# Kernel tuning notes

Hardware: AMD Instinct MI355X
Metric: run time of the kernel (lower is better)

The kernel has to match this reference:

```python
import jax, jax.numpy as jnp
import numpy as np

N_QUBITS = 13
DEPTH = 4
DIM = 2 ** N_QUBITS
PI = 3.141592653589793

# qubit 0 = most significant bit of the basis-state index
_idx = np.arange(DIM)
BITS = np.stack([(_idx >> (N_QUBITS - 1 - q)) & 1 for q in range(N_QUBITS)], axis=1)  # (DIM, n)
SIGNS = jnp.asarray(1.0 - 2.0 * BITS, dtype=jnp.float32)                               # Z eigenvalues, (DIM, n)
PARITY = jnp.asarray((-1.0) ** BITS.sum(axis=1), dtype=jnp.float32)                    # <Z^{(x)n}> diagonal, (DIM,)
# CZ entangling chain (q, q+1): diagonal (-1)^{sum_q b_q b_{q+1}}
ENT = jnp.asarray((-1.0) ** (BITS[:, :-1] * BITS[:, 1:]).sum(axis=1), dtype=jnp.float32)


def fwht(psi):
    """Normalized fast Walsh-Hadamard transform (H on every qubit), psi: (B, DIM) complex."""
    B = psi.shape[0]
    for q in range(N_QUBITS):
        psi = psi.reshape(B, 2 ** q, 2, -1)
        psi = jnp.stack([psi[:, :, 0] + psi[:, :, 1], psi[:, :, 0] - psi[:, :, 1]], axis=2)
    return psi.reshape(B, DIM) * (2.0 ** (-N_QUBITS / 2))


def feature_map_state(x):
    """Havlicek ZZ feature map: psi = D(x) H^n D(x) H^n |0...0>.
    Diagonal phase per basis state b: sum_j x_j s_j(b) + sum_{j<k} (pi-x_j)(pi-x_k) s_j(b) s_k(b)."""
    a = PI - x                                              # (B, n)
    u = x @ SIGNS.T                                         # (B, DIM)
    v = a @ SIGNS.T                                         # (B, DIM)
    phi = u + 0.5 * (v * v - jnp.sum(a * a, axis=1, keepdims=True))  # pair term via (sum)^2 trick
    d = jnp.exp(1j * phi)                                   # complex64 diagonal
    psi = jnp.full((x.shape[0], DIM), DIM ** -0.5, dtype=jnp.complex64)  # H^n |0>
    psi = fwht(d * psi)
    return d * psi


def _apply_1q(psi, U, q):
    """Apply 2x2 complex gate U to qubit q (bit-sliced)."""
    B = psi.shape[0]
    psi = psi.reshape(B, 2 ** q, 2, -1)
    a0, a1 = psi[:, :, 0], psi[:, :, 1]
    out = jnp.stack([U[0, 0] * a0 + U[0, 1] * a1, U[1, 0] * a0 + U[1, 1] * a1], axis=2)
    return out.reshape(B, DIM)


def variational_apply(psi, theta):
    """(DEPTH+1) layers of per-qubit Rz(b)Ry(a), CZ-chain entanglers between layers."""
    th = theta.reshape(DEPTH + 1, N_QUBITS, 2)
    for l in range(DEPTH + 1):
        if l > 0:
            psi = psi * ENT
        for q in range(N_QUBITS):
            ca = jnp.cos(0.5 * th[l, q, 0])
            sa = jnp.sin(0.5 * th[l, q, 0])
            em = jnp.exp(-0.5j * th[l, q, 1])
            ep = jnp.exp(0.5j * th[l, q, 1])
            U = jnp.stack([jnp.stack([em * ca, -em * sa]), jnp.stack([ep * sa, ep * ca])])
            psi = _apply_1q(psi, U, q)
    return psi


def setup_inputs() -> dict:
    key = jax.random.key(0)
    k1, k2 = jax.random.split(key)
    x = jax.random.normal(k1, (512, N_QUBITS), dtype=jnp.float32)
    theta = 0.1 * jax.random.normal(k2, ((DEPTH + 1) * N_QUBITS * 2,), dtype=jnp.float32)
    bias = jnp.zeros((1,), dtype=jnp.float32)
    return {"x": x, "theta": theta, "bias": bias}


def reference(x, theta, bias):
    psi = feature_map_state(x)
    psi = variational_apply(psi, theta)
    prob = psi.real ** 2 + psi.imag ** 2              # (B, DIM)
    logit = prob @ PARITY + bias[0]                   # (B,)
    return jnp.stack([-logit, logit], axis=1)         # two-class logits
```

## Files before the change

kernel.cpp:

```cpp
#include <hip/hip_runtime.h>
#include <hip/hip_fp16.h>

#define NQ   13
#define DIM  8192
#define PI_F 3.14159265358979323846f
#define NT   256
#define NAMP 32

#define NSLOT 9216

__device__ __forceinline__ int baseH(int t) { return 36 * t; }
__device__ __forceinline__ int baseL(int t) {
  int c = ((t & 1) << 7) | ((t & 2) << 5) | (t >> 2);
  return c + 4 * (c >> 5);
}

union F4H { float4 f; __half2 h[4]; };

__device__ __forceinline__ void rsincos(float x, float* s, float* c) {
  const float INV2PI = 0.15915494309189535f;
  const float TWOPI  = 6.283185307179586f;
  float r = x * INV2PI;
  r -= rintf(r);
  float ang = r * TWOPI;
  *s = __sinf(ang);
  *c = __cosf(ang);
}

__device__ __forceinline__ float2 f2fma(float s, float2 a, float2 b) {
  return make_float2(fmaf(s, a.x, b.x), fmaf(s, a.y, b.y));
}
__device__ __forceinline__ float2 f2add(float2 a, float2 b) {
  return make_float2(a.x + b.x, a.y + b.y);
}
__device__ __forceinline__ float2 f2sub(float2 a, float2 b) {
  return make_float2(a.x - b.x, a.y - b.y);
}
__device__ __forceinline__ float2 cphase(float2 v, float cs, float sn) {
  return make_float2(fmaf(cs, v.x, -sn * v.y), fmaf(cs, v.y, sn * v.x));
}
__device__ __forceinline__ float2 cmul(float2 a, float2 b) {
  return make_float2(fmaf(a.x, b.x, -a.y * b.y), fmaf(a.x, b.y, a.y * b.x));
}

template<int MASK>
__device__ __forceinline__ int xorLaneI(int x) {
  if constexpr (MASK == 1)
    return __builtin_amdgcn_update_dpp(x, x, 0xB1, 0xF, 0xF, false);
  else
    return __builtin_amdgcn_update_dpp(x, x, 0x4E, 0xF, 0xF, false);
}
template<int MASK>
__device__ __forceinline__ __half2 xorLaneH(__half2 v) {
  union { __half2 h; int i; } u; u.h = v;
  u.i = xorLaneI<MASK>(u.i);
  return u.h;
}

__device__ __forceinline__ void loadHh(const __half2* __restrict__ sAmp, int t, __half2* amp) {
  const __half2* p = sAmp + baseH(t);
  #pragma unroll
  for (int k = 0; k < 8; k++) {
    F4H u; u.f = *reinterpret_cast<const float4*>(p + 4 * k);
    #pragma unroll
    for (int c = 0; c < 4; c++) amp[4 * k + c] = u.h[c];
  }
}
__device__ __forceinline__ void storeHh(__half2* __restrict__ sAmp, int t, const __half2* amp) {
  __half2* p = sAmp + baseH(t);
  #pragma unroll
  for (int k = 0; k < 8; k++) {
    F4H u;
    #pragma unroll
    for (int c = 0; c < 4; c++) u.h[c] = amp[4 * k + c];
    *reinterpret_cast<float4*>(p + 4 * k) = u.f;
  }
}
__device__ __forceinline__ void loadLh(const __half2* __restrict__ sAmp, int t, __half2* amp) {
  const __half2* p = sAmp + baseL(t);
  #pragma unroll
  for (int j = 0; j < NAMP; j++) amp[j] = p[288 * j];
}
__device__ __forceinline__ void storeLh(__half2* __restrict__ sAmp, int t, const __half2* amp) {
  __half2* p = sAmp + baseL(t);
  #pragma unroll
  for (int j = 0; j < NAMP; j++) p[288 * j] = amp[j];
}

template<int KB>
__device__ __forceinline__ void fwht_bit(float2* amp) {
  #pragma unroll
  for (int j = 0; j < NAMP; j++) if (!(j & (1 << KB))) {
    int j1 = j | (1 << KB);
    float2 a0 = amp[j], a1 = amp[j1];
    amp[j]  = f2add(a0, a1);
    amp[j1] = f2sub(a0, a1);
  }
}
template<int KB>
__device__ __forceinline__ void applyRy(float2* amp, float ta, float sa) {
  #pragma unroll
  for (int j = 0; j < NAMP; j++) if (!(j & (1 << KB))) {
    int j1 = j | (1 << KB);
    amp[j]  = f2fma(-ta, amp[j1], amp[j]);
    amp[j1] = f2fma( sa, amp[j],  amp[j1]);
    amp[j]  = f2fma(-ta, amp[j1], amp[j]);
  }
}

template<int KB>
__device__ __forceinline__ void applyRyH(__half2* amp, __half2 nta, __half2 sa) {
  #pragma unroll
  for (int j = 0; j < NAMP; j++) if (!(j & (1 << KB))) {
    int j1 = j | (1 << KB);
    amp[j]  = __hfma2(nta, amp[j1], amp[j]);
    amp[j1] = __hfma2(sa,  amp[j],  amp[j1]);
    amp[j]  = __hfma2(nta, amp[j1], amp[j]);
  }
}

template<int MASK>
__device__ __forceinline__ void laneRyH(__half2* amp, __half2 c2, __half2 spm) {
  #pragma unroll
  for (int j = 0; j < NAMP; j++) {
    __half2 p = xorLaneH<MASK>(amp[j]);
    amp[j] = __hfma2(spm, p, __hmul2(c2, amp[j]));
  }
}
template<int MASK>
__device__ __forceinline__ void laneFwhtH(__half2* amp, __half2 sgn) {
  #pragma unroll
  for (int j = 0; j < NAMP; j++) {
    __half2 p = xorLaneH<MASK>(amp[j]);
    amp[j] = __hfma2(sgn, amp[j], p);
  }
}

template<int PAT>
__device__ __forceinline__ void buildTree(const float* __restrict__ w, float bias,
                                          int t, float* s) {
  float base = bias;
  if constexpr (PAT == 0) {
    #pragma unroll
    for (int k = 0; k < 8; k++) base += ((t >> k) & 1) ? w[5 + k] : 0.0f;
  } else {
    constexpr int BM[8] = {7, 6, 0, 1, 2, 3, 4, 5};
    #pragma unroll
    for (int k = 0; k < 8; k++) base += ((t >> k) & 1) ? w[BM[k]] : 0.0f;
  }
  constexpr int PH[5] = {0, 1, 2, 3, 4};
  constexpr int PL[5] = {8, 9, 10, 11, 12};
  s[0] = base;
  #pragma unroll
  for (int k = 0; k < 5; k++) {
    float wp = w[(PAT == 0) ? PH[k] : PL[k]];
    #pragma unroll
    for (int m = 0; m < (1 << k); m++) s[m | (1 << k)] = s[m] + wp;
  }
}

template<int PAT, bool INIT>
__device__ __forceinline__ void featureDiag(float2* amp,
                                            const float* __restrict__ wXp,
                                            const float* __restrict__ wAp,
                                            const float* __restrict__ consp, int t) {
  float u[NAMP], v[NAMP];
  buildTree<PAT>(wXp, consp[0], t, u);
  buildTree<PAT>(wAp, consp[1], t, v);
  float A2 = consp[2];
  #pragma unroll
  for (int j = 0; j < NAMP; j++) {
    float phi = u[j] + 0.5f * (v[j] * v[j] - A2);
    float sn, cs; rsincos(phi, &sn, &cs);
    if constexpr (INIT) amp[j] = make_float2(cs, sn);
    else                amp[j] = cphase(amp[j], cs, sn);
  }
}

template<int PAT>
__device__ __forceinline__ void applyDiag(float2* amp,
                                          const float* __restrict__ wb,
                                          const float* __restrict__ eR,
                                          const float* __restrict__ eI,
                                          float bias, int t) {
  float base = bias;
  if constexpr (PAT == 0) {
    #pragma unroll
    for (int k = 0; k < 8; k++) base += ((t >> k) & 1) ? wb[5 + k] : 0.0f;
  } else {
    constexpr int BM[8] = {7, 6, 0, 1, 2, 3, 4, 5};
    #pragma unroll
    for (int k = 0; k < 8; k++) base += ((t >> k) & 1) ? wb[BM[k]] : 0.0f;
  }
  constexpr int E0 = (PAT == 0) ? 0 : 8;
  const int ct = (PAT == 0) ? 0 : (((t & 1) << 7) | ((t & 2) << 5) | (t >> 2));
  float2 c[16];
  { float sn, cs; rsincos(base, &sn, &cs); c[0] = make_float2(cs, sn); }
  #pragma unroll
  for (int k = 0; k < 4; k++) {
    float2 e = make_float2(eR[E0 + k], eI[E0 + k]);
    #pragma unroll
    for (int m = 0; m < (1 << k); m++) c[m | (1 << k)] = cmul(c[m], e);
  }
  #pragma unroll
  for (int j = 0; j < 16; j++) {
    int i = (PAT == 0) ? ((t << 5) | j) : ((j << 8) | ct);
    float sgn = (__popc(i & (i >> 1)) & 1) ? -1.0f : 1.0f;
    amp[j] = cphase(amp[j], c[j].x * sgn, c[j].y * sgn);
  }
  float2 e4 = make_float2(eR[E0 + 4], eI[E0 + 4]);
  #pragma unroll
  for (int j = 16; j < 32; j++) {
    int i = (PAT == 0) ? ((t << 5) | j) : ((j << 8) | ct);
    float sgn = (__popc(i & (i >> 1)) & 1) ? -1.0f : 1.0f;
    float2 cc = cmul(c[j - 16], e4);
    amp[j] = cphase(amp[j], cc.x * sgn, cc.y * sgn);
  }
}

__global__ __launch_bounds__(NT, 1) void qc_kernel(
    const float* __restrict__ xin,
    const float* __restrict__ thin,
    const float* __restrict__ bin,
    float* __restrict__ out) {
  __shared__ alignas(16) __half2 sAmp[NSLOT];
  __shared__ float gTA[65], gSA[65];
  __shared__ __half2 hNTA[65], hSA[65];
  __shared__ __half2 hC2[65], hS2[65];
  __shared__ float gBbit[65];
  __shared__ float eBr[65], eBi[65];
  __shared__ float wX[13], wA[13];
  __shared__ float cons[8];
  __shared__ float red[NT / 64];

  const int t = threadIdx.x;
  const int lane = t & 63;
  const int b = blockIdx.x;

  if (t < NQ) {
    float xq = xin[b * NQ + t];
    float aq = PI_F - xq;
    wX[12 - t] = -2.0f * xq;
    wA[12 - t] = -2.0f * aq;
  }
  if (t < 65) {
    float av = thin[2 * t];
    float bv = thin[2 * t + 1];
    float ca = cosf(0.5f * av);
    float sa = sinf(0.5f * av);
    float ta = sa / (1.0f + ca);
    gTA[t] = ta;
    gSA[t] = sa;
    hNTA[t] = __float2half2_rn(-ta);
    hSA[t]  = __float2half2_rn(sa);
    hC2[t]  = __float2half2_rn(ca);
    hS2[t]  = __float2half2_rn(sa);
    int l = t / NQ, q = t % NQ;
    int s = l * NQ + (12 - q);
    gBbit[s] = bv;
    eBr[s] = cosf(bv);
    eBi[s] = sinf(bv);
  }
  __syncthreads();
  if (t == 0) {
    float X = 0.f, A = 0.f, A2 = 0.f;
    for (int p = 0; p < NQ; p++) {
      float xq = -0.5f * wX[p], aq = -0.5f * wA[p];
      X += xq; A += aq; A2 += aq * aq;
    }
    cons[0] = X; cons[1] = A; cons[2] = A2;
    for (int l = 0; l < 5; l++) {
      float s = 0.f;
      for (int p = 0; p < NQ; p++) s += gBbit[l * NQ + p];
      cons[3 + l] = -0.5f * s;
    }
  }
  __syncthreads();

  const __half2 P1 = __float2half2_rn(1.0f), M1 = __float2half2_rn(-1.0f);

  {
    float2 ampF[NAMP];
    featureDiag<0, true>(ampF, wX, wA, cons, t);
    fwht_bit<0>(ampF); fwht_bit<1>(ampF); fwht_bit<2>(ampF);
    fwht_bit<3>(ampF); fwht_bit<4>(ampF);
    __half2 ampH[NAMP];
    #pragma unroll
    for (int j = 0; j < NAMP; j++) ampH[j] = __float22half2_rn(ampF[j]);
    laneFwhtH<1>(ampH, (lane & 1) ? M1 : P1);
    laneFwhtH<2>(ampH, (lane & 2) ? M1 : P1);
    storeHh(sAmp, t, ampH);
  }
  __syncthreads();

  {
    __half2 ampH[NAMP];
    loadLh(sAmp, t, ampH);
    laneFwhtH<1>(ampH, (lane & 1) ? M1 : P1);
    float2 ampF[NAMP];
    #pragma unroll
    for (int j = 0; j < NAMP; j++) ampF[j] = __half22float2(ampH[j]);
    fwht_bit<0>(ampF); fwht_bit<1>(ampF); fwht_bit<2>(ampF);
    fwht_bit<3>(ampF); fwht_bit<4>(ampF);
    featureDiag<1, false>(ampF, wX, wA, cons, t);
    applyRy<2>(ampF, gTA[2], gSA[2]);
    applyRy<3>(ampF, gTA[1], gSA[1]);
    applyRy<4>(ampF, gTA[0], gSA[0]);
    #pragma unroll
    for (int j = 0; j < NAMP; j++) ampH[j] = __float22half2_rn(ampF[j]);
    applyRyH<0>(ampH, hNTA[4], hSA[4]);
    applyRyH<1>(ampH, hNTA[3], hSA[3]);
    { __half2 s2 = hS2[5];
      laneRyH<1>(ampH, hC2[5], (lane & 1) ? s2 : __hneg2(s2)); }
    storeLh(sAmp, t, ampH);
  }
  __syncthreads();

  for (int l = 0; l < 4; l += 2) {
    const int g = l * NQ, g1 = g + NQ, g2 = g1 + NQ;
    {
      __half2 ampH[NAMP];
      loadHh(sAmp, t, ampH);
      { __half2 s2 = hS2[g + 7];
        laneRyH<1>(ampH, hC2[g + 7], (lane & 1) ? s2 : __hneg2(s2)); }
      { __half2 s2 = hS2[g + 6];
        laneRyH<2>(ampH, hC2[g + 6], (lane & 2) ? s2 : __hneg2(s2)); }
      applyRyH<2>(ampH, hNTA[g + 10], hSA[g + 10]);
      applyRyH<3>(ampH, hNTA[g + 9],  hSA[g + 9]);
      applyRyH<4>(ampH, hNTA[g + 8],  hSA[g + 8]);
      float2 ampF[NAMP];
      #pragma unroll
      for (int j = 0; j < NAMP; j++) ampF[j] = __half22float2(ampH[j]);
      applyRy<0>(ampF, gTA[g + 12], gSA[g + 12]);
      applyRy<1>(ampF, gTA[g + 11], gSA[g + 11]);
      applyDiag<0>(ampF, gBbit + g, eBr + g, eBi + g, cons[3 + l], t);
      applyRy<0>(ampF, gTA[g1 + 12], gSA[g1 + 12]);
      applyRy<1>(ampF, gTA[g1 + 11], gSA[g1 + 11]);
      #pragma unroll
      for (int j = 0; j < NAMP; j++) ampH[j] = __float22half2_rn(ampF[j]);
      applyRyH<2>(ampH, hNTA[g1 + 10], hSA[g1 + 10]);
      applyRyH<3>(ampH, hNTA[g1 + 9],  hSA[g1 + 9]);
      applyRyH<4>(ampH, hNTA[g1 + 8],  hSA[g1 + 8]);
      { __half2 s2 = hS2[g1 + 7];
        laneRyH<1>(ampH, hC2[g1 + 7], (lane & 1) ? s2 : __hneg2(s2)); }
      { __half2 s2 = hS2[g1 + 6];
        laneRyH<2>(ampH, hC2[g1 + 6], (lane & 2) ? s2 : __hneg2(s2)); }
      storeHh(sAmp, t, ampH);
    }
    __syncthreads();
    {
      __half2 ampH[NAMP];
      loadLh(sAmp, t, ampH);
      { __half2 s2 = hS2[g1 + 5];
        laneRyH<1>(ampH, hC2[g1 + 5], (lane & 1) ? s2 : __hneg2(s2)); }
      applyRyH<0>(ampH, hNTA[g1 + 4], hSA[g1 + 4]);
      applyRyH<1>(ampH, hNTA[g1 + 3], hSA[g1 + 3]);
      float2 ampF[NAMP];
      #pragma unroll
      for (int j = 0; j < NAMP; j++) ampF[j] = __half22float2(ampH[j]);
      applyRy<2>(ampF, gTA[g1 + 2], gSA[g1 + 2]);
      applyRy<3>(ampF, gTA[g1 + 1], gSA[g1 + 1]);
      applyRy<4>(ampF, gTA[g1 + 0], gSA[g1 + 0]);
      applyDiag<1>(ampF, gBbit + g1, eBr + g1, eBi + g1, cons[3 + l + 1], t);
      applyRy<2>(ampF, gTA[g2 + 2], gSA[g2 + 2]);
      applyRy<3>(ampF, gTA[g2 + 1], gSA[g2 + 1]);
      applyRy<4>(ampF, gTA[g2 + 0], gSA[g2 + 0]);
      #pragma unroll
      for (int j = 0; j < NAMP; j++) ampH[j] = __float22half2_rn(ampF[j]);
      applyRyH<0>(ampH, hNTA[g2 + 4], hSA[g2 + 4]);
      applyRyH<1>(ampH, hNTA[g2 + 3], hSA[g2 + 3]);
      { __half2 s2 = hS2[g2 + 5];
        laneRyH<1>(ampH, hC2[g2 + 5], (lane & 1) ? s2 : __hneg2(s2)); }
      storeLh(sAmp, t, ampH);
    }
    __syncthreads();
  }

  float acc = 0.0f;
  {
    const int g = 4 * NQ;
    __half2 ampH[NAMP];
    loadHh(sAmp, t, ampH);
    { __half2 s2 = hS2[g + 7];
      laneRyH<1>(ampH, hC2[g + 7], (lane & 1) ? s2 : __hneg2(s2)); }
    { __half2 s2 = hS2[g + 6];
      laneRyH<2>(ampH, hC2[g + 6], (lane & 2) ? s2 : __hneg2(s2)); }
    applyRyH<2>(ampH, hNTA[g + 10], hSA[g + 10]);
    applyRyH<3>(ampH, hNTA[g + 9],  hSA[g + 9]);
    applyRyH<4>(ampH, hNTA[g + 8],  hSA[g + 8]);
    float2 ampF[NAMP];
    #pragma unroll
    for (int j = 0; j < NAMP; j++) ampF[j] = __half22float2(ampH[j]);
    applyRy<0>(ampF, gTA[g + 12], gSA[g + 12]);
    applyRy<1>(ampF, gTA[g + 11], gSA[g + 11]);
    int pt = __popc(t) & 1;
    #pragma unroll
    for (int j = 0; j < NAMP; j++) {
      float p2 = fmaf(ampF[j].x, ampF[j].x, ampF[j].y * ampF[j].y);
      acc += ((pt + __popc(j)) & 1) ? -p2 : p2;
    }
  }

  #pragma unroll
  for (int off = 32; off > 0; off >>= 1) acc += __shfl_down(acc, off, 64);
  if ((t & 63) == 0) red[t >> 6] = acc;
  __syncthreads();
  if (t == 0) {
    float total = red[0] + red[1] + red[2] + red[3];
    float logit = total * (1.0f / 67108864.0f) + bin[0];
    out[b * 2 + 0] = -logit;
    out[b * 2 + 1] = logit;
  }
}

extern "C" void kernel_launch(void* const* d_in, const int* in_sizes, int n_in,
                              void* d_out, int out_size, void* d_ws, size_t ws_size,
                              hipStream_t stream) {
  const float* x  = (const float*)d_in[0];
  const float* th = (const float*)d_in[1];
  const float* bi = (const float*)d_in[2];
  float* out = (float*)d_out;
  int B = in_sizes[0] / NQ;
  qc_kernel<<<B, NT, 0, stream>>>(x, th, bi, out);
}
```

Before: 91.23 us.

## Split state vector over 512 threads with 16 amplitudes each and new lane permutations

Doubles threads per block to 512 and halves per-thread amplitudes to 16, remapping which qubits live in registers, in DPP lane exchanges (adding a row-shift mask 8 partner), and in shared memory via new permH/permL index permutations. The half-precision in-register Ry path is removed, so more gates run in fp32 registers, and launch bounds now allow four blocks per CU. The aim is lower register pressure and higher occupancy to hide latency. In exchange it adds more cross-lane DPP ops, changes the LDS access patterns, and the row-shift DPP variant may not act as a true xor-8 exchange.

```diff
diff --git a/kernel.cpp b/kernel.cpp
--- a/kernel.cpp
+++ b/kernel.cpp
@@ -4,16 +4,19 @@
 #define NQ   13
 #define DIM  8192
 #define PI_F 3.14159265358979323846f
-#define NT   256
-#define NAMP 32
+#define NT   512
+#define NAMP 16
 
 #define NSLOT 9216
 
-__device__ __forceinline__ int baseH(int t) { return 36 * t; }
-__device__ __forceinline__ int baseL(int t) {
-  int c = ((t & 1) << 7) | ((t & 2) << 5) | (t >> 2);
-  return c + 4 * (c >> 5);
-}
+__device__ __forceinline__ int permH(int t) {
+  return (t & 0x1F3) | (((t >> 3) & 1) << 2) | (((t >> 2) & 1) << 3);
+}
+__device__ __forceinline__ int permL(int t) {
+  return ((t & 1) << 7) | (((t >> 1) & 1) << 8) | ((t >> 2) & 0x7F);
+}
+__device__ __forceinline__ int baseH(int g) { return 16 * g + 4 * (g >> 1); }
+__device__ __forceinline__ int baseL(int c) { return c + 4 * (c >> 5); }
 
 union F4H { float4 f; __half2 h[4]; };
 
@@ -44,47 +47,45 @@
 }
 
 template<int MASK>
-__device__ __forceinline__ int xorLaneI(int x) {
+__device__ __forceinline__ __half2 partnerH(__half2 v) {
+  union { __half2 h; int i; } u, r; u.h = v;
   if constexpr (MASK == 1)
-    return __builtin_amdgcn_update_dpp(x, x, 0xB1, 0xF, 0xF, false);
+    r.i = __builtin_amdgcn_update_dpp(u.i, u.i, 0xB1, 0xF, 0xF, false);
+  else if constexpr (MASK == 2)
+    r.i = __builtin_amdgcn_update_dpp(u.i, u.i, 0x4E, 0xF, 0xF, false);
   else
-    return __builtin_amdgcn_update_dpp(x, x, 0x4E, 0xF, 0xF, false);
-}
-template<int MASK>
-__device__ __forceinline__ __half2 xorLaneH(__half2 v) {
-  union { __half2 h; int i; } u; u.h = v;
-  u.i = xorLaneI<MASK>(u.i);
-  return u.h;
-}
-
-__device__ __forceinline__ void loadHh(const __half2* __restrict__ sAmp, int t, __half2* amp) {
-  const __half2* p = sAmp + baseH(t);
-  #pragma unroll
-  for (int k = 0; k < 8; k++) {
+    r.i = __builtin_amdgcn_update_dpp(u.i, u.i, 0x128, 0xF, 0xF, false);
+  return r.h;
+}
+
+__device__ __forceinline__ void loadHh(const __half2* __restrict__ sAmp, int g, __half2* amp) {
+  const __half2* p = sAmp + baseH(g);
+  #pragma unroll
+  for (int k = 0; k < 4; k++) {
     F4H u; u.f = *reinterpret_cast<const float4*>(p + 4 * k);
     #pragma unroll
     for (int c = 0; c < 4; c++) amp[4 * k + c] = u.h[c];
   }
 }
-__device__ __forceinline__ void storeHh(__half2* __restrict__ sAmp, int t, const __half2* amp) {
-  __half2* p = sAmp + baseH(t);
-  #pragma unroll
-  for (int k = 0; k < 8; k++) {
+__device__ __forceinline__ void storeHh(__half2* __restrict__ sAmp, int g, const __half2* amp) {
+  __half2* p = sAmp + baseH(g);
+  #pragma unroll
+  for (int k = 0; k < 4; k++) {
     F4H u;
     #pragma unroll
     for (int c = 0; c < 4; c++) u.h[c] = amp[4 * k + c];
     *reinterpret_cast<float4*>(p + 4 * k) = u.f;
   }
 }
-__device__ __forceinline__ void loadLh(const __half2* __restrict__ sAmp, int t, __half2* amp) {
-  const __half2* p = sAmp + baseL(t);
-  #pragma unroll
-  for (int j = 0; j < NAMP; j++) amp[j] = p[288 * j];
-}
-__device__ __forceinline__ void storeLh(__half2* __restrict__ sAmp, int t, const __half2* amp) {
-  __half2* p = sAmp + baseL(t);
-  #pragma unroll
-  for (int j = 0; j < NAMP; j++) p[288 * j] = amp[j];
+__device__ __forceinline__ void loadLh(const __half2* __restrict__ sAmp, int c, __half2* amp) {
+  const __half2* p = sAmp + baseL(c);
+  #pragma unroll
+  for (int j = 0; j < NAMP; j++) amp[j] = p[576 * j];
+}
+__device__ __forceinline__ void storeLh(__half2* __restrict__ sAmp, int c, const __half2* amp) {
+  __half2* p = sAmp + baseL(c);
+  #pragma unroll
+  for (int j = 0; j < NAMP; j++) p[576 * j] = amp[j];
 }
 
 template<int KB>
@@ -108,22 +109,11 @@
   }
 }
 
-template<int KB>
-__device__ __forceinline__ void applyRyH(__half2* amp, __half2 nta, __half2 sa) {
-  #pragma unroll
-  for (int j = 0; j < NAMP; j++) if (!(j & (1 << KB))) {
-    int j1 = j | (1 << KB);
-    amp[j]  = __hfma2(nta, amp[j1], amp[j]);
-    amp[j1] = __hfma2(sa,  amp[j],  amp[j1]);
-    amp[j]  = __hfma2(nta, amp[j1], amp[j]);
-  }
-}
-
 template<int MASK>
 __device__ __forceinline__ void laneRyH(__half2* amp, __half2 c2, __half2 spm) {
   #pragma unroll
   for (int j = 0; j < NAMP; j++) {
-    __half2 p = xorLaneH<MASK>(amp[j]);
+    __half2 p = partnerH<MASK>(amp[j]);
     amp[j] = __hfma2(spm, p, __hmul2(c2, amp[j]));
   }
 }
@@ -131,29 +121,23 @@
 __device__ __forceinline__ void laneFwhtH(__half2* amp, __half2 sgn) {
   #pragma unroll
   for (int j = 0; j < NAMP; j++) {
-    __half2 p = xorLaneH<MASK>(amp[j]);
+    __half2 p = partnerH<MASK>(amp[j]);
     amp[j] = __hfma2(sgn, amp[j], p);
   }
 }
 
 template<int PAT>
 __device__ __forceinline__ void buildTree(const float* __restrict__ w, float bias,
-                                          int t, float* s) {
+                                          int x, float* s) {
   float base = bias;
-  if constexpr (PAT == 0) {
-    #pragma unroll
-    for (int k = 0; k < 8; k++) base += ((t >> k) & 1) ? w[5 + k] : 0.0f;
-  } else {
-    constexpr int BM[8] = {7, 6, 0, 1, 2, 3, 4, 5};
-    #pragma unroll
-    for (int k = 0; k < 8; k++) base += ((t >> k) & 1) ? w[BM[k]] : 0.0f;
-  }
-  constexpr int PH[5] = {0, 1, 2, 3, 4};
-  constexpr int PL[5] = {8, 9, 10, 11, 12};
+  constexpr int B0 = (PAT == 0) ? 4 : 0;
+  #pragma unroll
+  for (int k = 0; k < 9; k++) base += ((x >> k) & 1) ? w[B0 + k] : 0.0f;
+  constexpr int W0 = (PAT == 0) ? 0 : 9;
   s[0] = base;
   #pragma unroll
-  for (int k = 0; k < 5; k++) {
-    float wp = w[(PAT == 0) ? PH[k] : PL[k]];
+  for (int k = 0; k < 4; k++) {
+    float wp = w[W0 + k];
     #pragma unroll
     for (int m = 0; m < (1 << k); m++) s[m | (1 << k)] = s[m] + wp;
   }
@@ -163,10 +147,10 @@
 __device__ __forceinline__ void featureDiag(float2* amp,
                                             const float* __restrict__ wXp,
                                             const float* __restrict__ wAp,
-                                            const float* __restrict__ consp, int t) {
+                                            const float* __restrict__ consp, int x) {
   float u[NAMP], v[NAMP];
-  buildTree<PAT>(wXp, consp[0], t, u);
-  buildTree<PAT>(wAp, consp[1], t, v);
+  buildTree<PAT>(wXp, consp[0], x, u);
+  buildTree<PAT>(wAp, consp[1], x, v);
   float A2 = consp[2];
   #pragma unroll
   for (int j = 0; j < NAMP; j++) {
@@ -182,50 +166,54 @@
                                           const float* __restrict__ wb,
                                           const float* __restrict__ eR,
                                           const float* __restrict__ eI,
-                                          float bias, int t) {
+                                          float bias, int x) {
   float base = bias;
-  if constexpr (PAT == 0) {
-    #pragma unroll
-    for (int k = 0; k < 8; k++) base += ((t >> k) & 1) ? wb[5 + k] : 0.0f;
-  } else {
-    constexpr int BM[8] = {7, 6, 0, 1, 2, 3, 4, 5};
-    #pragma unroll
-    for (int k = 0; k < 8; k++) base += ((t >> k) & 1) ? wb[BM[k]] : 0.0f;
-  }
-  constexpr int E0 = (PAT == 0) ? 0 : 8;
-  const int ct = (PAT == 0) ? 0 : (((t & 1) << 7) | ((t & 2) << 5) | (t >> 2));
+  constexpr int B0 = (PAT == 0) ? 4 : 0;
+  #pragma unroll
+  for (int k = 0; k < 9; k++) base += ((x >> k) & 1) ? wb[B0 + k] : 0.0f;
+  constexpr int W0 = (PAT == 0) ? 0 : 9;
   float2 c[16];
   { float sn, cs; rsincos(base, &sn, &cs); c[0] = make_float2(cs, sn); }
   #pragma unroll
   for (int k = 0; k < 4; k++) {
-    float2 e = make_float2(eR[E0 + k], eI[E0 + k]);
+    float2 e = make_float2(eR[W0 + k], eI[W0 + k]);
     #pragma unroll
     for (int m = 0; m < (1 << k); m++) c[m | (1 << k)] = cmul(c[m], e);
   }
+  const int st = __popc(x & (x >> 1)) & 1;
+  const int tb = (PAT == 0) ? (x & 1) : ((x >> 8) & 1);
   #pragma unroll
   for (int j = 0; j < 16; j++) {
-    int i = (PAT == 0) ? ((t << 5) | j) : ((j << 8) | ct);
-    float sgn = (__popc(i & (i >> 1)) & 1) ? -1.0f : 1.0f;
+    int jb = (PAT == 0) ? ((j >> 3) & 1) : (j & 1);
+    int sg = st ^ (jb & tb) ^ (__popc(j & (j >> 1)) & 1);
+    float sgn = sg ? -1.0f : 1.0f;
     amp[j] = cphase(amp[j], c[j].x * sgn, c[j].y * sgn);
   }
-  float2 e4 = make_float2(eR[E0 + 4], eI[E0 + 4]);
-  #pragma unroll
-  for (int j = 16; j < 32; j++) {
-    int i = (PAT == 0) ? ((t << 5) | j) : ((j << 8) | ct);
-    float sgn = (__popc(i & (i >> 1)) & 1) ? -1.0f : 1.0f;
-    float2 cc = cmul(c[j - 16], e4);
-    amp[j] = cphase(amp[j], cc.x * sgn, cc.y * sgn);
-  }
-}
-
-__global__ __launch_bounds__(NT, 1) void qc_kernel(
+}
+
+__device__ __forceinline__ void laneGatesH(__half2* ampH,
+                                           const __half2* __restrict__ hC2,
+                                           const __half2* __restrict__ hS2,
+                                           int g0, int lane) {
+  { __half2 s2 = hS2[g0 + 8]; laneRyH<1>(ampH, hC2[g0 + 8], (lane & 1) ? s2 : __hneg2(s2)); }
+  { __half2 s2 = hS2[g0 + 7]; laneRyH<2>(ampH, hC2[g0 + 7], (lane & 2) ? s2 : __hneg2(s2)); }
+  { __half2 s2 = hS2[g0 + 6]; laneRyH<8>(ampH, hC2[g0 + 6], (lane & 8) ? s2 : __hneg2(s2)); }
+}
+__device__ __forceinline__ void laneGatesL(__half2* ampH,
+                                           const __half2* __restrict__ hC2,
+                                           const __half2* __restrict__ hS2,
+                                           int g0, int lane) {
+  { __half2 s2 = hS2[g0 + 5]; laneRyH<1>(ampH, hC2[g0 + 5], (lane & 1) ? s2 : __hneg2(s2)); }
+  { __half2 s2 = hS2[g0 + 4]; laneRyH<2>(ampH, hC2[g0 + 4], (lane & 2) ? s2 : __hneg2(s2)); }
+}
+
+__global__ __launch_bounds__(NT, 4) void qc_kernel(
     const float* __restrict__ xin,
     const float* __restrict__ thin,
     const float* __restrict__ bin,
     float* __restrict__ out) {
   __shared__ alignas(16) __half2 sAmp[NSLOT];
   __shared__ float gTA[65], gSA[65];
-  __shared__ __half2 hNTA[65], hSA[65];
   __shared__ __half2 hC2[65], hS2[65];
   __shared__ float gBbit[65];
   __shared__ float eBr[65], eBi[65];
@@ -235,6 +223,8 @@
 
   const int t = threadIdx.x;
   const int lane = t & 63;
+  const int g = permH(t);
+  const int cc = permL(t);
   const int b = blockIdx.x;
 
   if (t < NQ) {
@@ -251,10 +241,8 @@
     float ta = sa / (1.0f + ca);
     gTA[t] = ta;
     gSA[t] = sa;
-    hNTA[t] = __float2half2_rn(-ta);
-    hSA[t]  = __float2half2_rn(sa);
-    hC2[t]  = __float2half2_rn(ca);
-    hS2[t]  = __float2half2_rn(sa);
+    hC2[t] = __float2half2_rn(ca);
+    hS2[t] = __float2half2_rn(sa);
     int l = t / NQ, q = t % NQ;
     int s = l * NQ + (12 - q);
     gBbit[s] = bv;
@@ -281,118 +269,100 @@
 
   {
     float2 ampF[NAMP];
-    featureDiag<0, true>(ampF, wX, wA, cons, t);
-    fwht_bit<0>(ampF); fwht_bit<1>(ampF); fwht_bit<2>(ampF);
-    fwht_bit<3>(ampF); fwht_bit<4>(ampF);
+    featureDiag<0, true>(ampF, wX, wA, cons, g);
+    fwht_bit<0>(ampF); fwht_bit<1>(ampF); fwht_bit<2>(ampF); fwht_bit<3>(ampF);
     __half2 ampH[NAMP];
     #pragma unroll
     for (int j = 0; j < NAMP; j++) ampH[j] = __float22half2_rn(ampF[j]);
     laneFwhtH<1>(ampH, (lane & 1) ? M1 : P1);
     laneFwhtH<2>(ampH, (lane & 2) ? M1 : P1);
-    storeHh(sAmp, t, ampH);
+    laneFwhtH<8>(ampH, (lane & 8) ? M1 : P1);
+    storeHh(sAmp, g, ampH);
   }
   __syncthreads();
 
   {
     __half2 ampH[NAMP];
-    loadLh(sAmp, t, ampH);
+    loadLh(sAmp, cc, ampH);
     laneFwhtH<1>(ampH, (lane & 1) ? M1 : P1);
+    laneFwhtH<2>(ampH, (lane & 2) ? M1 : P1);
     float2 ampF[NAMP];
     #pragma unroll
     for (int j = 0; j < NAMP; j++) ampF[j] = __half22float2(ampH[j]);
-    fwht_bit<0>(ampF); fwht_bit<1>(ampF); fwht_bit<2>(ampF);
-    fwht_bit<3>(ampF); fwht_bit<4>(ampF);
-    featureDiag<1, false>(ampF, wX, wA, cons, t);
-    applyRy<2>(ampF, gTA[2], gSA[2]);
-    applyRy<3>(ampF, gTA[1], gSA[1]);
-    applyRy<4>(ampF, gTA[0], gSA[0]);
+    fwht_bit<0>(ampF); fwht_bit<1>(ampF); fwht_bit<2>(ampF); fwht_bit<3>(ampF);
+    featureDiag<1, false>(ampF, wX, wA, cons, cc);
+    applyRy<0>(ampF, gTA[3], gSA[3]);
+    applyRy<1>(ampF, gTA[2], gSA[2]);
+    applyRy<2>(ampF, gTA[1], gSA[1]);
+    applyRy<3>(ampF, gTA[0], gSA[0]);
     #pragma unroll
     for (int j = 0; j < NAMP; j++) ampH[j] = __float22half2_rn(ampF[j]);
-    applyRyH<0>(ampH, hNTA[4], hSA[4]);
-    applyRyH<1>(ampH, hNTA[3], hSA[3]);
-    { __half2 s2 = hS2[5];
-      laneRyH<1>(ampH, hC2[5], (lane & 1) ? s2 : __hneg2(s2)); }
-    storeLh(sAmp, t, ampH);
+    laneGatesL(ampH, hC2, hS2, 0, lane);
+    storeLh(sAmp, cc, ampH);
   }
   __syncthreads();
 
   for (int l = 0; l < 4; l += 2) {
-    const int g = l * NQ, g1 = g + NQ, g2 = g1 + NQ;
+    const int ga = l * NQ, gb = ga + NQ, gc = gb + NQ;
     {
       __half2 ampH[NAMP];
-      loadHh(sAmp, t, ampH);
-      { __half2 s2 = hS2[g + 7];
-        laneRyH<1>(ampH, hC2[g + 7], (lane & 1) ? s2 : __hneg2(s2)); }
-      { __half2 s2 = hS2[g + 6];
-        laneRyH<2>(ampH, hC2[g + 6], (lane & 2) ? s2 : __hneg2(s2)); }
-      applyRyH<2>(ampH, hNTA[g + 10], hSA[g + 10]);
-      applyRyH<3>(ampH, hNTA[g + 9],  hSA[g + 9]);
-      applyRyH<4>(ampH, hNTA[g + 8],  hSA[g + 8]);
+      loadHh(sAmp, g, ampH);
+      laneGatesH(ampH, hC2, hS2, ga, lane);
       float2 ampF[NAMP];
       #pragma unroll
       for (int j = 0; j < NAMP; j++) ampF[j] = __half22float2(ampH[j]);
-      applyRy<0>(ampF, gTA[g + 12], gSA[g + 12]);
-      applyRy<1>(ampF, gTA[g + 11], gSA[g + 11]);
-      applyDiag<0>(ampF, gBbit + g, eBr + g, eBi + g, cons[3 + l], t);
-      applyRy<0>(ampF, gTA[g1 + 12], gSA[g1 + 12]);
-      applyRy<1>(ampF, gTA[g1 + 11], gSA[g1 + 11]);
+      applyRy<0>(ampF, gTA[ga + 12], gSA[ga + 12]);
+      applyRy<1>(ampF, gTA[ga + 11], gSA[ga + 11]);
+      applyRy<2>(ampF, gTA[ga + 10], gSA[ga + 10]);
+      applyRy<3>(ampF, gTA[ga + 9],  gSA[ga + 9]);
+      applyDiag<0>(ampF, gBbit + ga, eBr + ga, eBi + ga, cons[3 + l], g);
+      applyRy<0>(ampF, gTA[gb + 12], gSA[gb + 12]);
+      applyRy<1>(ampF, gTA[gb + 11], gSA[gb + 11]);
+      applyRy<2>(ampF, gTA[gb + 10], gSA[gb + 10]);
+      applyRy<3>(ampF, gTA[gb + 9],  gSA[gb + 9]);
       #pragma unroll
       for (int j = 0; j < NAMP; j++) ampH[j] = __float22half2_rn(ampF[j]);
-      applyRyH<2>(ampH, hNTA[g1 + 10], hSA[g1 + 10]);
-      applyRyH<3>(ampH, hNTA[g1 + 9],  hSA[g1 + 9]);
-      applyRyH<4>(ampH, hNTA[g1 + 8],  hSA[g1 + 8]);
-      { __half2 s2 = hS2[g1 + 7];
-        laneRyH<1>(ampH, hC2[g1 + 7], (lane & 1) ? s2 : __hneg2(s2)); }
-      { __half2 s2 = hS2[g1 + 6];
-        laneRyH<2>(ampH, hC2[g1 + 6], (lane & 2) ? s2 : __hneg2(s2)); }
-      storeHh(sAmp, t, ampH);
+      laneGatesH(ampH, hC2, hS2, gb, lane);
+      storeHh(sAmp, g, ampH);
     }
     __syncthreads();
     {
       __half2 ampH[NAMP];
-      loadLh(sAmp, t, ampH);
-      { __half2 s2 = hS2[g1 + 5];
-        laneRyH<1>(ampH, hC2[g1 + 5], (lane & 1) ? s2 : __hneg2(s2)); }
-      applyRyH<0>(ampH, hNTA[g1 + 4], hSA[g1 + 4]);
-      applyRyH<1>(ampH, hNTA[g1 + 3], hSA[g1 + 3]);
+      loadLh(sAmp, cc, ampH);
+      laneGatesL(ampH, hC2, hS2, gb, lane);
       float2 ampF[NAMP];
       #pragma unroll
       for (int j = 0; j < NAMP; j++) ampF[j] = __half22float2(ampH[j]);
-      applyRy<2>(ampF, gTA[g1 + 2], gSA[g1 + 2]);
-      applyRy<3>(ampF, gTA[g1 + 1], gSA[g1 + 1]);
-      applyRy<4>(ampF, gTA[g1 + 0], gSA[g1 + 0]);
-      applyDiag<1>(ampF, gBbit + g1, eBr + g1, eBi + g1, cons[3 + l + 1], t);
-      applyRy<2>(ampF, gTA[g2 + 2], gSA[g2 + 2]);
-      applyRy<3>(ampF, gTA[g2 + 1], gSA[g2 + 1]);
-      applyRy<4>(ampF, gTA[g2 + 0], gSA[g2 + 0]);
+      applyRy<0>(ampF, gTA[gb + 3], gSA[gb + 3]);
+      applyRy<1>(ampF, gTA[gb + 2], gSA[gb + 2]);
+      applyRy<2>(ampF, gTA[gb + 1], gSA[gb + 1]);
+      applyRy<3>(ampF, gTA[gb + 0], gSA[gb + 0]);
+      applyDiag<1>(ampF, gBbit + gb, eBr + gb, eBi + gb, cons[3 + l + 1], cc);
+      applyRy<0>(ampF, gTA[gc + 3], gSA[gc + 3]);
+      applyRy<1>(ampF, gTA[gc + 2], gSA[gc + 2]);
+      applyRy<2>(ampF, gTA[gc + 1], gSA[gc + 1]);
+      applyRy<3>(ampF, gTA[gc + 0], gSA[gc + 0]);
       #pragma unroll
       for (int j = 0; j < NAMP; j++) ampH[j] = __float22half2_rn(ampF[j]);
-      applyRyH<0>(ampH, hNTA[g2 + 4], hSA[g2 + 4]);
-      applyRyH<1>(ampH, hNTA[g2 + 3], hSA[g2 + 3]);
-      { __half2 s2 = hS2[g2 + 5];
-        laneRyH<1>(ampH, hC2[g2 + 5], (lane & 1) ? s2 : __hneg2(s2)); }
-      storeLh(sAmp, t, ampH);
+      laneGatesL(ampH, hC2, hS2, gc, lane);
+      storeLh(sAmp, cc, ampH);
     }
     __syncthreads();
   }
 
   float acc = 0.0f;
   {
-    const int g = 4 * NQ;
+    const int ga = 4 * NQ;
     __half2 ampH[NAMP];
-    loadHh(sAmp, t, ampH);
-    { __half2 s2 = hS2[g + 7];
-      laneRyH<1>(ampH, hC2[g + 7], (lane & 1) ? s2 : __hneg2(s2)); }
-    { __half2 s2 = hS2[g + 6];
-      laneRyH<2>(ampH, hC2[g + 6], (lane & 2) ? s2 : __hneg2(s2)); }
-    applyRyH<2>(ampH, hNTA[g + 10], hSA[g + 10]);
-    applyRyH<3>(ampH, hNTA[g + 9],  hSA[g + 9]);
-    applyRyH<4>(ampH, hNTA[g + 8],  hSA[g + 8]);
+    loadHh(sAmp, g, ampH);
+    laneGatesH(ampH, hC2, hS2, ga, lane);
     float2 ampF[NAMP];
     #pragma unroll
     for (int j = 0; j < NAMP; j++) ampF[j] = __half22float2(ampH[j]);
-    applyRy<0>(ampF, gTA[g + 12], gSA[g + 12]);
-    applyRy<1>(ampF, gTA[g + 11], gSA[g + 11]);
+    applyRy<0>(ampF, gTA[ga + 12], gSA[ga + 12]);
+    applyRy<1>(ampF, gTA[ga + 11], gSA[ga + 11]);
+    applyRy<2>(ampF, gTA[ga + 10], gSA[ga + 10]);
+    applyRy<3>(ampF, gTA[ga + 9],  gSA[ga + 9]);
     int pt = __popc(t) & 1;
     #pragma unroll
     for (int j = 0; j < NAMP; j++) {
@@ -406,7 +376,9 @@
   if ((t & 63) == 0) red[t >> 6] = acc;
   __syncthreads();
   if (t == 0) {
-    float total = red[0] + red[1] + red[2] + red[3];
+    float total = 0.f;
+    #pragma unroll
+    for (int w = 0; w < NT / 64; w++) total += red[w];
     float logit = total * (1.0f / 67108864.0f) + bin[0];
     out[b * 2 + 0] = -logit;
     out[b * 2 + 1] = logit;
```

Result: no change. 92.68 us (+1.6%).
